# Kernel tuning notes

Hardware: AMD Instinct MI355X
Metric: run time of the kernel (lower is better)

## Reference

```python
import jax, jax.numpy as jnp
import numpy as np

TAU = 2.0   # membrane decay time constant
TH = 1.0    # firing threshold

N, T, D = 64, 64, 8192


def setup_inputs() -> dict:
    key = jax.random.key(0)
    k1, k2, k3 = jax.random.split(key, 3)
    x = jax.random.normal(k1, (N, T, D), dtype=jnp.float32)
    momentum = jax.random.uniform(k2, (1,), dtype=jnp.float32)
    lamb = jax.random.uniform(k3, (1,), dtype=jnp.float32)
    return {"x": x, "momentum": momentum, "lamb": lamb}


def reference(x, momentum, lamb):
    """Momentum LIF neuron scanned over the time axis.

    Assumed dynamics (CUDA kernel source unavailable; reduces to standard
    STBP hard-reset LIF when momentum == 0 and lamb == 0):
        v_t = momentum * v_{t-1} + x_t - lamb * u_{t-1}   # momentum on input current
        u_t = (1 - 1/tau) * u_{t-1} + v_t                 # leaky integrate
        s_t = H(u_t - th)                                 # spike
        u_t = u_t * (1 - s_t)                             # hard reset
    x: [N, T, D] -> spikes: [N, T, D]
    """
    decay = 1.0 - 1.0 / TAU
    mom = momentum[0]
    lb = lamb[0]

    def step(carry, xt):
        u, v = carry                      # each [N, D]
        v = mom * v + xt - lb * u
        u = decay * u + v
        s = (u >= TH).astype(xt.dtype)
        u = u * (1.0 - s)                 # hard reset
        return (u, v), s

    xs = jnp.swapaxes(x, 0, 1)            # [T, N, D] for time scan
    u0 = jnp.zeros_like(x[:, 0])
    v0 = jnp.zeros_like(x[:, 0])
    _, spikes = jax.lax.scan(step, (u0, v0), xs)
    return jnp.swapaxes(spikes, 0, 1)      # [N, T, D]
```

## Files before the change

### kernel.cpp

```cpp
#include <hip/hip_runtime.h>


#define N_ 64
#define T_ 64
#define D_ 8192

__global__ __launch_bounds__(256) void MomentumLIF_kernel(
    const float* __restrict__ x,
    const float* __restrict__ momp,
    const float* __restrict__ lambp,
    float* __restrict__ out)
{
#pragma clang fp contract(off)
    const float mom  = momp[0];
    const float lamb = lambp[0];
    const float decay = 0.5f;

    const int tid = blockIdx.x * blockDim.x + threadIdx.x;
    const int n = tid >> 13;
    const int d = tid & (D_ - 1);

    const float* __restrict__ xp = x   + (size_t)n * T_ * D_ + d;
    float*       __restrict__ op = out + (size_t)n * T_ * D_ + d;

    float u = 0.f, v = 0.f;

#pragma unroll 8
    for (int t = 0; t < T_; ++t) {
        const float xt = xp[(size_t)t * D_];

        float t1 = mom * v;
        float t2 = lamb * u;
        v = (t1 + xt) - t2;
        u = decay * u + v;
        const bool sp = (u >= 1.0f);
        op[(size_t)t * D_] = sp ? 1.0f : 0.0f;
        u = sp ? 0.0f : u;
    }
}

extern "C" void kernel_launch(void* const* d_in, const int* in_sizes, int n_in,
                              void* d_out, int out_size, void* d_ws, size_t ws_size,
                              hipStream_t stream) {
    const float* x    = (const float*)d_in[0];
    const float* momp = (const float*)d_in[1];
    const float* lamb = (const float*)d_in[2];
    float* out = (float*)d_out;

    const int threads = N_ * D_;
    dim3 block(256);
    dim3 grid(threads / 256);
    hipLaunchKernelGGL(MomentumLIF_kernel, grid, block, 0, stream,
                       x, momp, lamb, out);
}
```

Measured before the change: 241.7 us.

## Software-prefetch inputs with inline asm and defer spike stores via bitmask

Loads the first 16 timesteps up front using inline global_load_dword and keeps a rolling 16-deep prefetch window with explicit s_waitcnt. Spikes are packed into two 32-bit masks and written out only after the recurrence finishes. The aim is to keep many loads in flight and take stores off the serial dependency chain. This adds register pressure and depends on hand-managed vmcnt accounting being correct.

```diff
diff --git a/kernel.cpp b/kernel.cpp
--- a/kernel.cpp
+++ b/kernel.cpp
@@ -1,9 +1,11 @@
 #include <hip/hip_runtime.h>
+#include <stdint.h>
 
 
 #define N_ 64
 #define T_ 64
 #define D_ 8192
+#define PF 16
 
 __global__ __launch_bounds__(256) void MomentumLIF_kernel(
     const float* __restrict__ x,
@@ -12,30 +14,71 @@
     float* __restrict__ out)
 {
 #pragma clang fp contract(off)
-    const float mom  = momp[0];
-    const float lamb = lambp[0];
+    float mom  = momp[0];
+    float lamb = lambp[0];
     const float decay = 0.5f;
+
+    asm volatile("" : "+s"(mom), "+s"(lamb));
 
     const int tid = blockIdx.x * blockDim.x + threadIdx.x;
     const int n = tid >> 13;
     const int d = tid & (D_ - 1);
 
-    const float* __restrict__ xp = x   + (size_t)n * T_ * D_ + d;
-    float*       __restrict__ op = out + (size_t)n * T_ * D_ + d;
+    const float* xp = x   + (size_t)n * T_ * D_ + d;
+    float*       op = out + (size_t)n * T_ * D_ + d;
+
+    float xs[PF];
+
+#pragma unroll
+    for (int i = 0; i < PF; ++i) {
+        const float* a = xp + (size_t)i * D_;
+        asm volatile("global_load_dword %0, %1, off" : "=v"(xs[i]) : "v"(a));
+    }
 
     float u = 0.f, v = 0.f;
+    uint32_t blo = 0u, bhi = 0u;
 
-#pragma unroll 8
-    for (int t = 0; t < T_; ++t) {
-        const float xt = xp[(size_t)t * D_];
+#pragma unroll
+    for (int t = 0; t < T_ - PF; ++t) {
+        const int slot = t & (PF - 1);
+        asm volatile("s_waitcnt vmcnt(15)" : "+v"(xs[slot]));
+        const float xt = xs[slot];
+        const float* a = xp + (size_t)(t + PF) * D_;
+        asm volatile("global_load_dword %0, %1, off" : "=v"(xs[slot]) : "v"(a));
 
         float t1 = mom * v;
         float t2 = lamb * u;
         v = (t1 + xt) - t2;
         u = decay * u + v;
         const bool sp = (u >= 1.0f);
-        op[(size_t)t * D_] = sp ? 1.0f : 0.0f;
+        if (t < 32) blo |= ((uint32_t)sp) << t;
+        else        bhi |= ((uint32_t)sp) << (t - 32);
         u = sp ? 0.0f : u;
+    }
+
+    asm volatile("s_waitcnt vmcnt(0)"
+                 : "+v"(xs[0]),  "+v"(xs[1]),  "+v"(xs[2]),  "+v"(xs[3]),
+                   "+v"(xs[4]),  "+v"(xs[5]),  "+v"(xs[6]),  "+v"(xs[7]),
+                   "+v"(xs[8]),  "+v"(xs[9]),  "+v"(xs[10]), "+v"(xs[11]),
+                   "+v"(xs[12]), "+v"(xs[13]), "+v"(xs[14]), "+v"(xs[15]));
+
+#pragma unroll
+    for (int t = T_ - PF; t < T_; ++t) {
+        const float xt = xs[t & (PF - 1)];
+        float t1 = mom * v;
+        float t2 = lamb * u;
+        v = (t1 + xt) - t2;
+        u = decay * u + v;
+        const bool sp = (u >= 1.0f);
+        if (t < 32) blo |= ((uint32_t)sp) << t;
+        else        bhi |= ((uint32_t)sp) << (t - 32);
+        u = sp ? 0.0f : u;
+    }
+
+#pragma unroll
+    for (int t = 0; t < T_; ++t) {
+        const uint32_t bit = ((t < 32 ? blo : bhi) >> (t & 31)) & 1u;
+        op[(size_t)t * D_] = bit ? 1.0f : 0.0f;
     }
 }
 
```

After: 234.6 us. -2.9%, faster.

## Stream inputs via async global-to-LDS ring buffer and defer spike stores

Applied to the files above, without the earlier changes.

Loads the x time series through a 16-deep LDS ring buffer using global_load_lds direct-to-shared copies with explicit vmcnt waits, so up to 16 timesteps of loads are in flight while the recurrence runs. Spikes are packed into two 32-bit bitmasks and written out in a separate loop after the scan, which keeps stores out of the dependent chain. In exchange it uses LDS, relies on hand-tuned vmcnt counts that are easy to get wrong, and delays all stores to the end of the kernel.

```diff
diff --git a/kernel.cpp b/kernel.cpp
--- a/kernel.cpp
+++ b/kernel.cpp
@@ -1,9 +1,15 @@
 #include <hip/hip_runtime.h>
+#include <stdint.h>
 
 
 #define N_ 64
 #define T_ 64
 #define D_ 8192
+#define RS 16
+#define CHK 8
+
+typedef __attribute__((address_space(1))) uint32_t* gptr_t;
+typedef __attribute__((address_space(3))) uint32_t* lptr_t;
 
 __global__ __launch_bounds__(256) void MomentumLIF_kernel(
     const float* __restrict__ x,
@@ -12,30 +18,66 @@
     float* __restrict__ out)
 {
 #pragma clang fp contract(off)
+    __shared__ uint32_t smem[RS * 256];
+
     const float mom  = momp[0];
     const float lamb = lambp[0];
     const float decay = 0.5f;
 
-    const int tid = blockIdx.x * blockDim.x + threadIdx.x;
-    const int n = tid >> 13;
-    const int d = tid & (D_ - 1);
+    const int tid = threadIdx.x;
+    const int blk = blockIdx.x;
+    const int n   = blk >> 5;
+    const int d   = ((blk & 31) << 8) + tid;
+    const int wbase = tid & 192;
 
-    const float* __restrict__ xp = x   + (size_t)n * T_ * D_ + d;
-    float*       __restrict__ op = out + (size_t)n * T_ * D_ + d;
+    const uint32_t* xrow = reinterpret_cast<const uint32_t*>(x)
+                         + (size_t)n * T_ * D_ + d;
+    float* op = out + (size_t)n * T_ * D_ + d;
+
+    asm volatile("s_waitcnt vmcnt(0)" ::: "memory");
+
+#define STAGE(t_) __builtin_amdgcn_global_load_lds(                       \
+        (gptr_t)(xrow + (size_t)(t_) * D_),                               \
+        (lptr_t)(&smem[(((t_) & (RS - 1)) << 8) + wbase]), 4, 0, 0)
+
+#pragma unroll
+    for (int t = 0; t < RS; ++t) STAGE(t);
 
     float u = 0.f, v = 0.f;
+    uint32_t blo = 0u, bhi = 0u;
 
-#pragma unroll 8
+#pragma unroll
+    for (int c = 0; c < T_ / CHK; ++c) {
+        if (c < 7) asm volatile("s_waitcnt vmcnt(8)" ::: "memory");
+        else       asm volatile("s_waitcnt vmcnt(0)" ::: "memory");
+
+#pragma unroll
+        for (int i = 0; i < CHK; ++i) {
+            const int t = c * CHK + i;
+            const float xt =
+                __uint_as_float(smem[((t & (RS - 1)) << 8) + tid]);
+
+            float t1 = mom * v;
+            float t2 = lamb * u;
+            v = (t1 + xt) - t2;
+            u = decay * u + v;
+            const bool sp = (u >= 1.0f);
+            if (t < 32) blo |= ((uint32_t)sp) << t;
+            else        bhi |= ((uint32_t)sp) << (t - 32);
+            u = sp ? 0.0f : u;
+        }
+
+        if (c < 6) {
+#pragma unroll
+            for (int i = 0; i < CHK; ++i) STAGE(RS + c * CHK + i);
+        }
+    }
+#undef STAGE
+
+#pragma unroll
     for (int t = 0; t < T_; ++t) {
-        const float xt = xp[(size_t)t * D_];
-
-        float t1 = mom * v;
-        float t2 = lamb * u;
-        v = (t1 + xt) - t2;
-        u = decay * u + v;
-        const bool sp = (u >= 1.0f);
-        op[(size_t)t * D_] = sp ? 1.0f : 0.0f;
-        u = sp ? 0.0f : u;
+        const uint32_t bit = ((t < 32 ? blo : bhi) >> (t & 31)) & 1u;
+        op[(size_t)t * D_] = bit ? 1.0f : 0.0f;
     }
 }
 
```

New measurement: 233.7 us. -3.3%, faster.
